# Kernel tuning notes

Measured on AMD Instinct MI355X. Metric: run time of the kernel, lower is better.

The kernel has to match this reference:

```python
import jax, jax.numpy as jnp
import numpy as np

V, C, T, H, L, B = 32000, 1024, 1024, 16, 8, 4
HS = C // H
STD = 0.02


def _layernorm(x, g, b, eps=1e-5):
    m = jnp.mean(x, axis=-1, keepdims=True)
    v = jnp.mean(jnp.square(x - m), axis=-1, keepdims=True)
    return (x - m) * jax.lax.rsqrt(v + eps) * g + b


def setup_inputs() -> dict:
    key = jax.random.key(0)
    ks = jax.random.split(key, 16)
    n = lambda k, shape: (jax.random.normal(k, shape, dtype=jnp.float32) * STD)
    return {
        "index": jax.random.randint(ks[0], (B, T), 0, V),
        "targets": jax.random.randint(ks[1], (B, T), 0, V),
        "tok_emb": n(ks[2], (V, C)),
        "pos_emb": n(ks[3], (T, C)),
        "wq": n(ks[4], (L, C, C)),
        "wk": n(ks[5], (L, C, C)),
        "wv": n(ks[6], (L, C, C)),
        "wo": n(ks[7], (L, C, C)),
        "bo": jnp.zeros((L, C), jnp.float32),
        "w1": n(ks[8], (L, C, 4 * C)),
        "b1": jnp.zeros((L, 4 * C), jnp.float32),
        "w2": n(ks[9], (L, 4 * C, C)),
        "b2": jnp.zeros((L, C), jnp.float32),
        "ln1_g": jnp.ones((L, C), jnp.float32),
        "ln1_b": jnp.zeros((L, C), jnp.float32),
        "ln2_g": jnp.ones((L, C), jnp.float32),
        "ln2_b": jnp.zeros((L, C), jnp.float32),
        "lnf_g": jnp.ones((C,), jnp.float32),
        "lnf_b": jnp.zeros((C,), jnp.float32),
        "lm_w": n(ks[10], (C, V)),
        "lm_b": jnp.zeros((V,), jnp.float32),
    }


def reference(index, targets, tok_emb, pos_emb, wq, wk, wv, wo, bo, w1, b1, w2,
              b2, ln1_g, ln1_b, ln2_g, ln2_b, lnf_g, lnf_b, lm_w, lm_b):
    b, t = index.shape
    x = tok_emb[index] + pos_emb[:t]                      # [B,T,C]
    causal = jnp.tril(jnp.ones((t, t), dtype=bool))       # tril mask
    scale = HS ** -0.5
    for l in range(L):  # fixed small layer loop
        q = (x @ wq[l]).reshape(b, t, H, HS)
        k = (x @ wk[l]).reshape(b, t, H, HS)
        v = (x @ wv[l]).reshape(b, t, H, HS)
        scores = jnp.einsum('bqhd,bkhd->bhqk', q, k) * scale
        scores = jnp.where(causal, scores, -jnp.inf)
        w = jax.nn.softmax(scores, axis=-1)               # dropout p=0 -> identity
        att = jnp.einsum('bhqk,bkhd->bqhd', w, v).reshape(b, t, C)
        x = _layernorm(x + att @ wo[l] + bo[l], ln1_g[l], ln1_b[l])
        h = jax.nn.relu(x @ w1[l] + b1[l])
        x = _layernorm(x + h @ w2[l] + b2[l], ln2_g[l], ln2_b[l])
    x = _layernorm(x, lnf_g, lnf_b)
    logits = (x @ lm_w + lm_b).reshape(b * t, V)
    logp = jax.nn.log_softmax(logits, axis=-1)
    loss = -jnp.take_along_axis(logp, targets.reshape(-1, 1), axis=1).mean()
    return logits, loss
```

## Files before the change

### kernel.cpp

```cpp
#include <hip/hip_runtime.h>

typedef unsigned short u16;
typedef __attribute__((ext_vector_type(4))) float f32x4;
typedef __attribute__((ext_vector_type(8))) short s16x8;

static constexpr int V = 32000;
static constexpr int C = 1024;
static constexpr int T = 1024;
static constexpr int H = 16;
static constexpr int L = 8;
static constexpr int B = 4;
static constexpr int HS = 64;
static constexpr int BT = B * T;
static constexpr int C4 = 4 * C;
static constexpr int C3 = 3 * C;

__device__ __forceinline__ u16 f2bf(float f) {
  union { float f; unsigned u; } v; v.f = f;
  unsigned r = v.u + 0x7fffu + ((v.u >> 16) & 1u);
  return (u16)(r >> 16);
}

__device__ __forceinline__ void gload16(const u16* g, u16* l) {
  __builtin_amdgcn_global_load_lds(
      (const __attribute__((address_space(1))) void*)g,
      (__attribute__((address_space(3))) void*)l, 16, 0, 0);
}

__device__ __forceinline__ float blockReduceSum(float v) {
  __shared__ float red[4];
  int lane = threadIdx.x & 63, w = threadIdx.x >> 6;
#pragma unroll
  for (int m = 32; m >= 1; m >>= 1) v += __shfl_xor(v, m, 64);
  if (lane == 0) red[w] = v;
  __syncthreads();
  float r = red[0] + red[1] + red[2] + red[3];
  __syncthreads();
  return r;
}

__global__ __launch_bounds__(256) void k_embed(
    const int* __restrict__ idx, const float* __restrict__ tok,
    const float* __restrict__ pos, float* __restrict__ x, u16* __restrict__ xb) {
  int bt = blockIdx.x;
  int t = bt & (T - 1);
  int row = idx[bt];
  const float* te = tok + (size_t)row * C;
  const float* pe = pos + (size_t)t * C;
  float* xo = x + (size_t)bt * C;
  u16* xbo = xb + (size_t)bt * C;
  for (int c = threadIdx.x; c < C; c += 256) {
    float v = te[c] + pe[c];
    xo[c] = v;
    xbo[c] = f2bf(v);
  }
}

__global__ __launch_bounds__(256) void k_transpose(
    const float* __restrict__ W, u16* __restrict__ Wt, int K, int N,
    size_t sW, size_t sWt) {
  __shared__ float tile[64][65];
  const float* Wz = W + sW * blockIdx.z;
  u16* Wtz = Wt + sWt * blockIdx.z;
  int n0 = blockIdx.x * 64, k0 = blockIdx.y * 64;
  int tc = threadIdx.x & 63, tr = threadIdx.x >> 6;
#pragma unroll
  for (int i = 0; i < 16; ++i) {
    int r = tr + i * 4;
    tile[r][tc] = Wz[(size_t)(k0 + r) * N + (n0 + tc)];
  }
  __syncthreads();
#pragma unroll
  for (int i = 0; i < 16; ++i) {
    int r = tr + i * 4;
    Wtz[(size_t)(n0 + r) * K + (k0 + tc)] = f2bf(tile[tc][r]);
  }
}

__global__ __launch_bounds__(256) void k_vtrans(
    const u16* __restrict__ qkv, u16* __restrict__ vt) {
  __shared__ u16 tile[64][72];
  int bid = blockIdx.x;
  int tc = bid & 15, h = (bid >> 4) & 15, b = bid >> 8;
  int t0 = tc * 64;
  const size_t base = (size_t)b * T * C3 + 2 * C + (size_t)h * HS;
  int tid = threadIdx.x;
  int r = tid >> 3, c8 = (tid & 7) * 8;
#pragma unroll
  for (int it = 0; it < 2; ++it) {
    int row = r + it * 32;
    *(s16x8*)&tile[row][c8] =
        *(const s16x8*)&qkv[base + (size_t)(t0 + row) * C3 + c8];
  }
  __syncthreads();
  const size_t vbase = (size_t)(b * H + h) * HS * T + t0;
#pragma unroll
  for (int it = 0; it < 2; ++it) {
    int d = (tid >> 3) + it * 32;
    s16x8 o;
#pragma unroll
    for (int j = 0; j < 8; ++j) o[j] = (short)tile[c8 + j][d];
    *(s16x8*)&vt[vbase + (size_t)d * T + c8] = o;
  }
}

template <int OUT_BF16, int RELU, int HAS_BIAS, int HAS_RES>
__global__ __launch_bounds__(256, 2) void k_gemm(
    const u16* __restrict__ A, const u16* __restrict__ Bt,
    const float* __restrict__ bias, const float* __restrict__ Res,
    float* __restrict__ Cf, u16* __restrict__ Cb, int M, int N, int K) {
  __shared__ u16 As[128 * 32];
  __shared__ u16 Bs[128 * 32];
  int tid = threadIdx.x;
  int lane = tid & 63, wid = tid >> 6;
  int lm = lane & 15, lg = lane >> 4;
  int wm = wid >> 1, wn = wid & 1;

  unsigned nbx = gridDim.x;
  unsigned nwg = nbx * gridDim.y;
  unsigned orig = blockIdx.y * nbx + blockIdx.x;
  unsigned f = ((nwg & 7u) == 0u) ? (orig & 7u) * (nwg >> 3) + (orig >> 3) : orig;
  int mb = (int)(f / nbx) * 128, nb = (int)(f % nbx) * 128;

  f32x4 acc[4][4];
#pragma unroll
  for (int i = 0; i < 4; ++i)
#pragma unroll
    for (int j = 0; j < 4; ++j) acc[i][j] = f32x4{0.f, 0.f, 0.f, 0.f};

  int r0 = tid >> 2, q0 = tid & 3;
  int r1 = (256 + tid) >> 2, q1 = tid & 3;
  const u16* a0 = A + (size_t)(mb + r0) * K + q0 * 8;
  const u16* a1 = A + (size_t)(mb + r1) * K + q1 * 8;
  const u16* b0 = Bt + (size_t)(nb + r0) * K + q0 * 8;
  const u16* b1 = Bt + (size_t)(nb + r1) * K + q1 * 8;
  u16* lA0 = &As[wid * 512];
  u16* lA1 = &As[2048 + wid * 512];
  u16* lB0 = &Bs[wid * 512];
  u16* lB1 = &Bs[2048 + wid * 512];

  int nK = K >> 5;
  for (int kb = 0; kb < nK; ++kb) {
    __syncthreads();
    int ko = kb * 32;
    gload16(a0 + ko, lA0);
    gload16(a1 + ko, lA1);
    gload16(b0 + ko, lB0);
    gload16(b1 + ko, lB1);
    __syncthreads();
    s16x8 af[4], bfr[4];
#pragma unroll
    for (int m = 0; m < 4; ++m)
      af[m] = *(const s16x8*)&As[(wm * 64 + m * 16 + lm) * 32 + lg * 8];
#pragma unroll
    for (int n = 0; n < 4; ++n)
      bfr[n] = *(const s16x8*)&Bs[(wn * 64 + n * 16 + lm) * 32 + lg * 8];
#pragma unroll
    for (int m = 0; m < 4; ++m)
#pragma unroll
      for (int n = 0; n < 4; ++n)
        acc[m][n] = __builtin_amdgcn_mfma_f32_16x16x32_bf16(af[m], bfr[n],
                                                            acc[m][n], 0, 0, 0);
  }
#pragma unroll
  for (int m = 0; m < 4; ++m) {
#pragma unroll
    for (int n = 0; n < 4; ++n) {
      int col = nb + wn * 64 + n * 16 + lm;
      float bv = HAS_BIAS ? bias[col] : 0.0f;
#pragma unroll
      for (int r = 0; r < 4; ++r) {
        int row = mb + wm * 64 + m * 16 + lg * 4 + r;
        float v = acc[m][n][r] + bv;
        if (HAS_RES) v += Res[(size_t)row * N + col];
        if (RELU) v = v > 0.f ? v : 0.f;
        if (OUT_BF16)
          Cb[(size_t)row * N + col] = f2bf(v);
        else
          Cf[(size_t)row * N + col] = v;
      }
    }
  }
}

template <int OUT_BF16, int RELU, int HAS_BIAS, int HAS_RES>
__global__ __launch_bounds__(512) void k_gemm256(
    const u16* __restrict__ A, const u16* __restrict__ Bt,
    const float* __restrict__ bias, const float* __restrict__ Res,
    float* __restrict__ Cf, u16* __restrict__ Cb, int M, int N, int K) {
  __shared__ u16 As[2][16384];
  __shared__ u16 Bs[2][16384];
  const int tid = threadIdx.x;
  const int lane = tid & 63, wid = tid >> 6;
  const int lm = lane & 15, lg = lane >> 4;
  const int wr = wid >> 2, wc = wid & 3;

  unsigned nbx = gridDim.x;
  unsigned nwg = nbx * gridDim.y;
  unsigned orig = blockIdx.y * nbx + blockIdx.x;
  unsigned f = ((nwg & 7u) == 0u) ? (orig & 7u) * (nwg >> 3) + (orig >> 3) : orig;
  const int mb = (int)(f / nbx) * 256, nb = (int)(f % nbx) * 256;

  int aoff[4], boff[4], ldso[4];
#pragma unroll
  for (int h = 0; h < 4; ++h) {
    const int kk = h >> 1, p = h & 1;
    int rem = p * 512 + tid;
    int rblk = rem >> 6;
    int rem2 = rem & 63;
    int row16 = rem2 >> 2, psl = rem2 & 3;
    int sl = psl ^ ((row16 >> 1) & 3);
    int grow = rblk * 16 + row16;
    int gk = kk * 32 + sl * 8;
    aoff[h] = (mb + grow) * K + gk;
    boff[h] = (nb + grow) * K + gk;
    ldso[h] = kk * 8192 + p * 4096 + wid * 512;
  }
  const int lo = lm * 32 + ((lg ^ ((lm >> 1) & 3)) << 3);

  f32x4 acc[8][4];
#pragma unroll
  for (int i = 0; i < 8; ++i)
#pragma unroll
    for (int j = 0; j < 4; ++j) acc[i][j] = f32x4{0.f, 0.f, 0.f, 0.f};

  const int nK = K >> 6;
  gload16(A + aoff[0], &As[0][ldso[0]]);
  gload16(A + aoff[1], &As[0][ldso[1]]);
  gload16(Bt + boff[0], &Bs[0][ldso[0]]);
  gload16(Bt + boff[1], &Bs[0][ldso[1]]);
  gload16(A + aoff[2], &As[0][ldso[2]]);
  gload16(A + aoff[3], &As[0][ldso[3]]);
  gload16(Bt + boff[2], &Bs[0][ldso[2]]);
  gload16(Bt + boff[3], &Bs[0][ldso[3]]);
  asm volatile("s_waitcnt vmcnt(4)" ::: "memory");
  __builtin_amdgcn_s_barrier();

  for (int t = 0; t < nK; ++t) {
    const int buf = t & 1, nbuf = buf ^ 1;
    const bool pre = (t + 1 < nK);
    const int nk64 = (t + 1) * 64;
    s16x8 af[4], bfr[4];
#pragma unroll
    for (int m = 0; m < 4; ++m)
      af[m] = *(const s16x8*)&As[buf][(wr * 8 + m) * 512 + lo];
#pragma unroll
    for (int n = 0; n < 4; ++n)
      bfr[n] = *(const s16x8*)&Bs[buf][(wc * 4 + n) * 512 + lo];
    if (pre) {
      gload16(A + aoff[0] + nk64, &As[nbuf][ldso[0]]);
      gload16(A + aoff[1] + nk64, &As[nbuf][ldso[1]]);
    }
    __builtin_amdgcn_s_barrier();
    __builtin_amdgcn_s_setprio(1);
#pragma unroll
    for (int m = 0; m < 4; ++m)
#pragma unroll
      for (int n = 0; n < 4; ++n)
        acc[m][n] = __builtin_amdgcn_mfma_f32_16x16x32_bf16(af[m], bfr[n],
                                                            acc[m][n], 0, 0, 0);
    __builtin_amdgcn_s_setprio(0);
    __builtin_amdgcn_s_barrier();
#pragma unroll
    for (int m = 0; m < 4; ++m)
      af[m] = *(const s16x8*)&As[buf][(wr * 8 + 4 + m) * 512 + lo];
    if (pre) {
      gload16(Bt + boff[0] + nk64, &Bs[nbuf][ldso[0]]);
      gload16(Bt + boff[1] + nk64, &Bs[nbuf][ldso[1]]);
    }
    __builtin_amdgcn_s_barrier();
    __builtin_amdgcn_s_setprio(1);
#pragma unroll
    for (int m = 0; m < 4; ++m)
#pragma unroll
      for (int n = 0; n < 4; ++n)
        acc[m + 4][n] = __builtin_amdgcn_mfma_f32_16x16x32_bf16(
            af[m], bfr[n], acc[m + 4][n], 0, 0, 0);
    __builtin_amdgcn_s_setprio(0);
    __builtin_amdgcn_s_barrier();
#pragma unroll
    for (int m = 0; m < 4; ++m)
      af[m] = *(const s16x8*)&As[buf][8192 + (wr * 8 + m) * 512 + lo];
#pragma unroll
    for (int n = 0; n < 4; ++n)
      bfr[n] = *(const s16x8*)&Bs[buf][8192 + (wc * 4 + n) * 512 + lo];
    if (pre) {
      gload16(A + aoff[2] + nk64, &As[nbuf][ldso[2]]);
      gload16(A + aoff[3] + nk64, &As[nbuf][ldso[3]]);
      asm volatile("s_waitcnt vmcnt(6)" ::: "memory");
    } else {
      asm volatile("s_waitcnt vmcnt(0)" ::: "memory");
    }
    __builtin_amdgcn_s_barrier();
    __builtin_amdgcn_s_setprio(1);
#pragma unroll
    for (int m = 0; m < 4; ++m)
#pragma unroll
      for (int n = 0; n < 4; ++n)
        acc[m][n] = __builtin_amdgcn_mfma_f32_16x16x32_bf16(af[m], bfr[n],
                                                            acc[m][n], 0, 0, 0);
    __builtin_amdgcn_s_setprio(0);
    __builtin_amdgcn_s_barrier();
#pragma unroll
    for (int m = 0; m < 4; ++m)
      af[m] = *(const s16x8*)&As[buf][8192 + (wr * 8 + 4 + m) * 512 + lo];
    if (pre) {
      gload16(Bt + boff[2] + nk64, &Bs[nbuf][ldso[2]]);
      gload16(Bt + boff[3] + nk64, &Bs[nbuf][ldso[3]]);
      asm volatile("s_waitcnt vmcnt(4)" ::: "memory");
    }
    __builtin_amdgcn_s_barrier();
    __builtin_amdgcn_s_setprio(1);
#pragma unroll
    for (int m = 0; m < 4; ++m)
#pragma unroll
      for (int n = 0; n < 4; ++n)
        acc[m + 4][n] = __builtin_amdgcn_mfma_f32_16x16x32_bf16(
            af[m], bfr[n], acc[m + 4][n], 0, 0, 0);
    __builtin_amdgcn_s_setprio(0);
    __builtin_amdgcn_s_barrier();
  }
  float bv[4];
#pragma unroll
  for (int n = 0; n < 4; ++n)
    bv[n] = HAS_BIAS ? bias[nb + wc * 64 + n * 16 + lm] : 0.0f;
#pragma unroll
  for (int m = 0; m < 8; ++m) {
#pragma unroll
    for (int r = 0; r < 4; ++r) {
      int row = mb + wr * 128 + m * 16 + lg * 4 + r;
#pragma unroll
      for (int n = 0; n < 4; ++n) {
        int col = nb + wc * 64 + n * 16 + lm;
        float v = acc[m][n][r] + bv[n];
        if (HAS_RES) v += Res[(size_t)row * N + col];
        if (RELU) v = v > 0.f ? v : 0.f;
        if (OUT_BF16)
          Cb[(size_t)row * N + col] = f2bf(v);
        else
          Cf[(size_t)row * N + col] = v;
      }
    }
  }
}

__global__ __launch_bounds__(256) void k_attn(
    const u16* __restrict__ qkv, const u16* __restrict__ vt,
    u16* __restrict__ o) {
  constexpr int PP = 72;
  __shared__ u16 Ks[64 * 64];
  __shared__ u16 Vs[64 * 64];
  __shared__ u16 Ps[4][16 * PP];
  int bid = blockIdx.x;
  int qt = bid & 15, h = (bid >> 4) & 15, b = bid >> 8;
  int tid = threadIdx.x, lane = tid & 63, wid = tid >> 6;
  int lm = lane & 15, lg = lane >> 4;
  const size_t rowbase = (size_t)b * T * C3 + (size_t)h * HS;
  const u16* kbase = qkv + rowbase + C;
  const u16* vbase = vt + (size_t)(b * H + h) * HS * T;
  int qb = qt * 64;
  int qw = qb + wid * 16;
  const float scale = 0.125f;

  s16x8 qf[2];
#pragma unroll
  for (int s = 0; s < 2; ++s)
    qf[s] = *(const s16x8*)&qkv[rowbase + (size_t)(qw + lm) * C3 + s * 32 + lg * 8];

  float m_[4], l_[4];
  f32x4 oacc[4];
#pragma unroll
  for (int r = 0; r < 4; ++r) { m_[r] = -3e38f; l_[r] = 0.f; }
#pragma unroll
  for (int n = 0; n < 4; ++n) oacc[n] = f32x4{0.f, 0.f, 0.f, 0.f};

  const int sr = tid >> 3, scs = (tid & 7) ^ (sr & 7);
  const int swz0 = ((lg) ^ (lm & 7)) * 8;
  const int swz1 = ((4 + lg) ^ (lm & 7)) * 8;

  for (int kt = 0; kt <= qt; ++kt) {
    __syncthreads();
    gload16(kbase + (size_t)(kt * 64 + sr) * C3 + scs * 8, &Ks[wid * 512]);
    gload16(kbase + (size_t)(kt * 64 + sr + 32) * C3 + scs * 8,
            &Ks[2048 + wid * 512]);
    gload16(vbase + (size_t)sr * T + kt * 64 + scs * 8, &Vs[wid * 512]);
    gload16(vbase + (size_t)(sr + 32) * T + kt * 64 + scs * 8,
            &Vs[2048 + wid * 512]);
    __syncthreads();

    f32x4 s[4];
#pragma unroll
    for (int ch = 0; ch < 4; ++ch) s[ch] = f32x4{0.f, 0.f, 0.f, 0.f};
#pragma unroll
    for (int ch = 0; ch < 4; ++ch) {
      s16x8 k0 = *(const s16x8*)&Ks[(ch * 16 + lm) * 64 + swz0];
      s16x8 k1 = *(const s16x8*)&Ks[(ch * 16 + lm) * 64 + swz1];
      s[ch] = __builtin_amdgcn_mfma_f32_16x16x32_bf16(qf[0], k0, s[ch], 0, 0, 0);
      s[ch] = __builtin_amdgcn_mfma_f32_16x16x32_bf16(qf[1], k1, s[ch], 0, 0, 0);
    }
    if (kt == qt) {
#pragma unroll
      for (int ch = 0; ch < 4; ++ch) {
        int col = kt * 64 + ch * 16 + lm;
#pragma unroll
        for (int r = 0; r < 4; ++r) {
          int row = qw + lg * 4 + r;
          s[ch][r] = (col <= row) ? s[ch][r] * scale : -3e38f;
        }
      }
    } else {
#pragma unroll
      for (int ch = 0; ch < 4; ++ch)
#pragma unroll
        for (int r = 0; r < 4; ++r) s[ch][r] *= scale;
    }
    float rmax[4];
#pragma unroll
    for (int r = 0; r < 4; ++r)
      rmax[r] = fmaxf(fmaxf(s[0][r], s[1][r]), fmaxf(s[2][r], s[3][r]));
#pragma unroll
    for (int mm = 1; mm < 16; mm <<= 1)
#pragma unroll
      for (int r = 0; r < 4; ++r)
        rmax[r] = fmaxf(rmax[r], __shfl_xor(rmax[r], mm, 16));
    float alpha[4], rsum[4];
#pragma unroll
    for (int r = 0; r < 4; ++r) {
      float mn = fmaxf(m_[r], rmax[r]);
      alpha[r] = __expf(m_[r] - mn);
      m_[r] = mn;
      rsum[r] = 0.f;
    }
#pragma unroll
    for (int ch = 0; ch < 4; ++ch)
#pragma unroll
      for (int r = 0; r < 4; ++r) {
        float e = __expf(s[ch][r] - m_[r]);
        s[ch][r] = e;
        rsum[r] += e;
      }
#pragma unroll
    for (int mm = 1; mm < 16; mm <<= 1)
#pragma unroll
      for (int r = 0; r < 4; ++r) rsum[r] += __shfl_xor(rsum[r], mm, 16);
#pragma unroll
    for (int r = 0; r < 4; ++r) l_[r] = l_[r] * alpha[r] + rsum[r];
#pragma unroll
    for (int n = 0; n < 4; ++n)
#pragma unroll
      for (int r = 0; r < 4; ++r) oacc[n][r] *= alpha[r];
#pragma unroll
    for (int r = 0; r < 4; ++r) {
      int pr = lg * 4 + r;
#pragma unroll
      for (int ch = 0; ch < 4; ++ch)
        Ps[wid][pr * PP + ch * 16 + lm] = f2bf(s[ch][r]);
    }
    s16x8 pa0 = *(const s16x8*)&Ps[wid][lm * PP + lg * 8];
    s16x8 pa1 = *(const s16x8*)&Ps[wid][lm * PP + 32 + lg * 8];
#pragma unroll
    for (int n = 0; n < 4; ++n) {
      s16x8 v0 = *(const s16x8*)&Vs[(n * 16 + lm) * 64 + swz0];
      s16x8 v1 = *(const s16x8*)&Vs[(n * 16 + lm) * 64 + swz1];
      oacc[n] = __builtin_amdgcn_mfma_f32_16x16x32_bf16(pa0, v0, oacc[n], 0, 0, 0);
      oacc[n] = __builtin_amdgcn_mfma_f32_16x16x32_bf16(pa1, v1, oacc[n], 0, 0, 0);
    }
  }
  const size_t obase = (size_t)b * T * C + (size_t)h * HS;
  float inv[4];
#pragma unroll
  for (int r = 0; r < 4; ++r) inv[r] = 1.0f / l_[r];
#pragma unroll
  for (int n = 0; n < 4; ++n)
#pragma unroll
    for (int r = 0; r < 4; ++r)
      o[obase + (size_t)(qw + lg * 4 + r) * C + n * 16 + lm] =
          f2bf(oacc[n][r] * inv[r]);
}

__global__ __launch_bounds__(256) void k_ln(
    const float* __restrict__ in, const float* __restrict__ g,
    const float* __restrict__ bsh, float* __restrict__ xout,
    u16* __restrict__ xbout) {
  int row = blockIdx.x;
  const float* xr = in + (size_t)row * C;
  int tid = threadIdx.x;
  float vals[4];
  float s = 0.f;
#pragma unroll
  for (int i = 0; i < 4; ++i) {
    float vv = xr[tid + i * 256];
    vals[i] = vv;
    s += vv;
  }
  s = blockReduceSum(s);
  float mean = s * (1.0f / C);
  float s2 = 0.f;
#pragma unroll
  for (int i = 0; i < 4; ++i) {
    float d = vals[i] - mean;
    s2 += d * d;
  }
  s2 = blockReduceSum(s2);
  float rstd = rsqrtf(s2 * (1.0f / C) + 1e-5f);
#pragma unroll
  for (int i = 0; i < 4; ++i) {
    int c = tid + i * 256;
    float y = (vals[i] - mean) * rstd * g[c] + bsh[c];
    xout[(size_t)row * C + c] = y;
    xbout[(size_t)row * C + c] = f2bf(y);
  }
}

__global__ __launch_bounds__(256) void k_rowloss(
    const float* __restrict__ logits, const int* __restrict__ tgt,
    float* __restrict__ rowloss) {
  int row = blockIdx.x;
  const float* lr = logits + (size_t)row * V;
  const f32x4* lr4 = (const f32x4*)lr;
  int tid = threadIdx.x;
  float m = -3e38f, s = 0.f;
  for (int i = tid; i < V / 4; i += 256) {
    f32x4 v = lr4[i];
#pragma unroll
    for (int j = 0; j < 4; ++j) {
      float x = v[j];
      if (x > m) {
        s = s * __expf(m - x) + 1.f;
        m = x;
      } else {
        s += __expf(x - m);
      }
    }
  }
#pragma unroll
  for (int d = 1; d < 64; d <<= 1) {
    float mo = __shfl_xor(m, d, 64), so = __shfl_xor(s, d, 64);
    float mn = fmaxf(m, mo);
    s = s * __expf(m - mn) + so * __expf(mo - mn);
    m = mn;
  }
  __shared__ float sm[4], ss[4];
  int w = tid >> 6;
  if ((tid & 63) == 0) { sm[w] = m; ss[w] = s; }
  __syncthreads();
  if (tid == 0) {
    float M = fmaxf(fmaxf(sm[0], sm[1]), fmaxf(sm[2], sm[3]));
    float S = ss[0] * __expf(sm[0] - M) + ss[1] * __expf(sm[1] - M) +
              ss[2] * __expf(sm[2] - M) + ss[3] * __expf(sm[3] - M);
    rowloss[row] = (M + logf(S)) - lr[tgt[row]];
  }
}

__global__ __launch_bounds__(256) void k_lossreduce(
    const float* __restrict__ rowloss, float* __restrict__ out) {
  __shared__ float red[256];
  int tid = threadIdx.x;
  float s = 0.f;
  for (int i = tid; i < BT; i += 256) s += rowloss[i];
  red[tid] = s;
  __syncthreads();
  for (int m = 128; m >= 1; m >>= 1) {
    if (tid < m) red[tid] += red[tid + m];
    __syncthreads();
  }
  if (tid == 0) out[0] = red[0] * (1.0f / BT);
}

extern "C" void kernel_launch(void* const* d_in, const int* in_sizes, int n_in,
                              void* d_out, int out_size, void* d_ws,
                              size_t ws_size, hipStream_t stream) {
  (void)in_sizes; (void)n_in; (void)out_size; (void)ws_size;
  const int* index = (const int*)d_in[0];
  const int* targets = (const int*)d_in[1];
  const float* tok_emb = (const float*)d_in[2];
  const float* pos_emb = (const float*)d_in[3];
  const float* wq = (const float*)d_in[4];
  const float* wk = (const float*)d_in[5];
  const float* wv = (const float*)d_in[6];
  const float* wo = (const float*)d_in[7];
  const float* bo = (const float*)d_in[8];
  const float* w1 = (const float*)d_in[9];
  const float* b1 = (const float*)d_in[10];
  const float* w2 = (const float*)d_in[11];
  const float* b2 = (const float*)d_in[12];
  const float* ln1_g = (const float*)d_in[13];
  const float* ln1_b = (const float*)d_in[14];
  const float* ln2_g = (const float*)d_in[15];
  const float* ln2_b = (const float*)d_in[16];
  const float* lnf_g = (const float*)d_in[17];
  const float* lnf_b = (const float*)d_in[18];
  const float* lm_w = (const float*)d_in[19];
  const float* lm_b = (const float*)d_in[20];

  float* logits = (float*)d_out;
  float* loss = logits + (size_t)BT * V;

  size_t off = 0;
  auto alloc = [&](size_t bytes) -> void* {
    off = (off + 255) & ~(size_t)255;
    void* p = (void*)((char*)d_ws + off);
    off += bytes;
    return p;
  };
  u16* wqkv_t = (u16*)alloc((size_t)L * C3 * C * 2);
  u16* wo_t = (u16*)alloc((size_t)L * C * C * 2);
  u16* w1_t = (u16*)alloc((size_t)L * C * C4 * 2);
  u16* w2_t = (u16*)alloc((size_t)L * C4 * C * 2);
  u16* lmw_t = (u16*)alloc((size_t)V * C * 2);
  float* x = (float*)alloc((size_t)BT * C * 4);
  float* tmp = (float*)alloc((size_t)BT * C * 4);
  u16* xb = (u16*)alloc((size_t)BT * C * 2);
  u16* qkvb = (u16*)alloc((size_t)BT * C3 * 2);
  u16* vtb = (u16*)alloc((size_t)BT * C * 2);
  u16* attb = (u16*)alloc((size_t)BT * C * 2);
  u16* hb = (u16*)alloc((size_t)BT * C4 * 2);
  float* rowloss = (float*)alloc((size_t)BT * 4);

  dim3 blk(256);
  dim3 blk5(512);
  k_transpose<<<dim3(C / 64, C / 64, L), blk, 0, stream>>>(
      wq, wqkv_t, C, C, (size_t)C * C, (size_t)C3 * C);
  k_transpose<<<dim3(C / 64, C / 64, L), blk, 0, stream>>>(
      wk, wqkv_t + (size_t)C * C, C, C, (size_t)C * C, (size_t)C3 * C);
  k_transpose<<<dim3(C / 64, C / 64, L), blk, 0, stream>>>(
      wv, wqkv_t + (size_t)2 * C * C, C, C, (size_t)C * C, (size_t)C3 * C);
  k_transpose<<<dim3(C / 64, C / 64, L), blk, 0, stream>>>(
      wo, wo_t, C, C, (size_t)C * C, (size_t)C * C);
  k_transpose<<<dim3(C4 / 64, C / 64, L), blk, 0, stream>>>(
      w1, w1_t, C, C4, (size_t)C * C4, (size_t)C * C4);
  k_transpose<<<dim3(C / 64, C4 / 64, L), blk, 0, stream>>>(
      w2, w2_t, C4, C, (size_t)C4 * C, (size_t)C4 * C);
  k_transpose<<<dim3(V / 64, C / 64, 1), blk, 0, stream>>>(
      lm_w, lmw_t, C, V, 0, 0);

  k_embed<<<BT, blk, 0, stream>>>(index, tok_emb, pos_emb, x, xb);

  dim3 gQKV(C3 / 128, BT / 128);
  dim3 gCC(C / 128, BT / 128);
  dim3 gC4(C4 / 256, BT / 256);
  for (int l = 0; l < L; ++l) {
    const u16* wqkvt = wqkv_t + (size_t)l * C3 * C;
    const u16* wot = wo_t + (size_t)l * C * C;
    const u16* w1t = w1_t + (size_t)l * C * C4;
    const u16* w2t = w2_t + (size_t)l * C4 * C;

    k_gemm<1, 0, 0, 0><<<gQKV, blk, 0, stream>>>(
        xb, wqkvt, nullptr, nullptr, nullptr, qkvb, BT, C3, C);
    k_vtrans<<<B * H * (T / 64), blk, 0, stream>>>(qkvb, vtb);
    k_attn<<<B * H * (T / 64), blk, 0, stream>>>(qkvb, vtb, attb);
    k_gemm<0, 0, 1, 1><<<gCC, blk, 0, stream>>>(
        attb, wot, bo + (size_t)l * C, x, tmp, nullptr, BT, C, C);
    k_ln<<<BT, blk, 0, stream>>>(tmp, ln1_g + (size_t)l * C,
                                 ln1_b + (size_t)l * C, x, xb);
    k_gemm256<1, 1, 1, 0><<<gC4, blk5, 0, stream>>>(
        xb, w1t, b1 + (size_t)l * C4, nullptr, nullptr, hb, BT, C4, C);
    k_gemm<0, 0, 1, 1><<<gCC, blk, 0, stream>>>(
        hb, w2t, b2 + (size_t)l * C, x, tmp, nullptr, BT, C, C4);
    k_ln<<<BT, blk, 0, stream>>>(tmp, ln2_g + (size_t)l * C,
                                 ln2_b + (size_t)l * C, x, xb);
  }
  k_ln<<<BT, blk, 0, stream>>>(x, lnf_g, lnf_b, x, xb);
  k_gemm256<0, 0, 1, 0><<<dim3(V / 256, BT / 256), blk5, 0, stream>>>(
      xb, lmw_t, lm_b, nullptr, logits, nullptr, BT, V, C);
  k_rowloss<<<BT, blk, 0, stream>>>(logits, targets, rowloss);
  k_lossreduce<<<1, blk, 0, stream>>>(rowloss, loss);
}
```

Baseline: 2.947 ms.

## Fuse V-transpose into QKV GEMM, balance causal attention, fuse loss partials into LM head

Several ideas land together. The QKV projection now runs on the 256-tile GEMM, whose epilogue writes V directly in transposed layout, so the separate transpose kernel is gone. Attention blocks each take a pair of query tiles (p and 15-p) to even out the causal workload. The LM-head GEMM epilogue computes per-tile row max and sum-exp partials, so the row-loss kernel only reduces 125 pairs instead of rereading all logits. These remove a kernel launch and a large logits reread, at the cost of more epilogue work and extra syncs in the GEMM.

```diff
diff --git a/kernel.cpp b/kernel.cpp
--- a/kernel.cpp
+++ b/kernel.cpp
@@ -3,6 +3,7 @@
 typedef unsigned short u16;
 typedef __attribute__((ext_vector_type(4))) float f32x4;
 typedef __attribute__((ext_vector_type(8))) short s16x8;
+typedef __attribute__((ext_vector_type(4))) short s16x4;
 
 static constexpr int V = 32000;
 static constexpr int C = 1024;
@@ -77,33 +78,6 @@
   }
 }
 
-__global__ __launch_bounds__(256) void k_vtrans(
-    const u16* __restrict__ qkv, u16* __restrict__ vt) {
-  __shared__ u16 tile[64][72];
-  int bid = blockIdx.x;
-  int tc = bid & 15, h = (bid >> 4) & 15, b = bid >> 8;
-  int t0 = tc * 64;
-  const size_t base = (size_t)b * T * C3 + 2 * C + (size_t)h * HS;
-  int tid = threadIdx.x;
-  int r = tid >> 3, c8 = (tid & 7) * 8;
-#pragma unroll
-  for (int it = 0; it < 2; ++it) {
-    int row = r + it * 32;
-    *(s16x8*)&tile[row][c8] =
-        *(const s16x8*)&qkv[base + (size_t)(t0 + row) * C3 + c8];
-  }
-  __syncthreads();
-  const size_t vbase = (size_t)(b * H + h) * HS * T + t0;
-#pragma unroll
-  for (int it = 0; it < 2; ++it) {
-    int d = (tid >> 3) + it * 32;
-    s16x8 o;
-#pragma unroll
-    for (int j = 0; j < 8; ++j) o[j] = (short)tile[c8 + j][d];
-    *(s16x8*)&vt[vbase + (size_t)d * T + c8] = o;
-  }
-}
-
 template <int OUT_BF16, int RELU, int HAS_BIAS, int HAS_RES>
 __global__ __launch_bounds__(256, 2) void k_gemm(
     const u16* __restrict__ A, const u16* __restrict__ Bt,
@@ -183,11 +157,12 @@
   }
 }
 
-template <int OUT_BF16, int RELU, int HAS_BIAS, int HAS_RES>
+template <int OUT_BF16, int RELU, int HAS_BIAS, int HAS_RES, int VT, int LOSS>
 __global__ __launch_bounds__(512) void k_gemm256(
     const u16* __restrict__ A, const u16* __restrict__ Bt,
     const float* __restrict__ bias, const float* __restrict__ Res,
-    float* __restrict__ Cf, u16* __restrict__ Cb, int M, int N, int K) {
+    float* __restrict__ Cf, u16* __restrict__ Cb, u16* __restrict__ Vtp,
+    float2* __restrict__ Pp, int M, int N, int K) {
   __shared__ u16 As[2][16384];
   __shared__ u16 Bs[2][16384];
   const int tid = threadIdx.x;
@@ -320,6 +295,24 @@
     __builtin_amdgcn_s_setprio(0);
     __builtin_amdgcn_s_barrier();
   }
+  if (VT && nb >= 2 * C) {
+    int hh = ((nb - 2 * C) >> 6) + wc;
+#pragma unroll
+    for (int m = 0; m < 8; ++m) {
+      int t0 = mb + wr * 128 + m * 16 + lg * 4;
+      int bb = t0 >> 10, tt = t0 & (T - 1);
+      size_t vbase = ((size_t)(bb * H + hh) * HS) * T + tt;
+#pragma unroll
+      for (int n = 0; n < 4; ++n) {
+        int d = n * 16 + lm;
+        s16x4 pk;
+#pragma unroll
+        for (int r = 0; r < 4; ++r) pk[r] = (short)f2bf(acc[m][n][r]);
+        *(s16x4*)&Vtp[vbase + (size_t)d * T] = pk;
+      }
+    }
+    return;
+  }
   float bv[4];
 #pragma unroll
   for (int n = 0; n < 4; ++n)
@@ -342,6 +335,80 @@
       }
     }
   }
+  if (LOSS) {
+    __syncthreads();
+    float* red = (float*)&As[0][0];
+    float Mx[8][4], Sx[8][4];
+#pragma unroll
+    for (int m = 0; m < 8; ++m)
+#pragma unroll
+      for (int r = 0; r < 4; ++r) {
+        float v0 = acc[m][0][r] + bv[0];
+        float v1 = acc[m][1][r] + bv[1];
+        float v2 = acc[m][2][r] + bv[2];
+        float v3 = acc[m][3][r] + bv[3];
+        Mx[m][r] = fmaxf(fmaxf(v0, v1), fmaxf(v2, v3));
+      }
+#pragma unroll
+    for (int d = 1; d < 16; d <<= 1)
+#pragma unroll
+      for (int m = 0; m < 8; ++m)
+#pragma unroll
+        for (int r = 0; r < 4; ++r)
+          Mx[m][r] = fmaxf(Mx[m][r], __shfl_xor(Mx[m][r], d, 16));
+    if (lm == 0) {
+#pragma unroll
+      for (int m = 0; m < 8; ++m)
+#pragma unroll
+        for (int r = 0; r < 4; ++r)
+          red[(wr * 128 + m * 16 + lg * 4 + r) * 4 + wc] = Mx[m][r];
+    }
+    __syncthreads();
+#pragma unroll
+    for (int m = 0; m < 8; ++m)
+#pragma unroll
+      for (int r = 0; r < 4; ++r) {
+        int rl = wr * 128 + m * 16 + lg * 4 + r;
+        Mx[m][r] = fmaxf(fmaxf(red[rl * 4 + 0], red[rl * 4 + 1]),
+                         fmaxf(red[rl * 4 + 2], red[rl * 4 + 3]));
+      }
+    __syncthreads();
+#pragma unroll
+    for (int m = 0; m < 8; ++m)
+#pragma unroll
+      for (int r = 0; r < 4; ++r)
+        Sx[m][r] = __expf(acc[m][0][r] + bv[0] - Mx[m][r]) +
+                   __expf(acc[m][1][r] + bv[1] - Mx[m][r]) +
+                   __expf(acc[m][2][r] + bv[2] - Mx[m][r]) +
+                   __expf(acc[m][3][r] + bv[3] - Mx[m][r]);
+#pragma unroll
+    for (int d = 1; d < 16; d <<= 1)
+#pragma unroll
+      for (int m = 0; m < 8; ++m)
+#pragma unroll
+        for (int r = 0; r < 4; ++r)
+          Sx[m][r] += __shfl_xor(Sx[m][r], d, 16);
+    if (lm == 0) {
+#pragma unroll
+      for (int m = 0; m < 8; ++m)
+#pragma unroll
+        for (int r = 0; r < 4; ++r)
+          red[(wr * 128 + m * 16 + lg * 4 + r) * 4 + wc] = Sx[m][r];
+    }
+    __syncthreads();
+    if (wc == 0 && lm == 0) {
+      int nblk = nb >> 8;
+#pragma unroll
+      for (int m = 0; m < 8; ++m)
+#pragma unroll
+        for (int r = 0; r < 4; ++r) {
+          int rl = wr * 128 + m * 16 + lg * 4 + r;
+          float ss = red[rl * 4 + 0] + red[rl * 4 + 1] + red[rl * 4 + 2] +
+                     red[rl * 4 + 3];
+          Pp[(size_t)(mb + rl) * 128 + nblk] = float2{Mx[m][r], ss};
+        }
+    }
+  }
 }
 
 __global__ __launch_bounds__(256) void k_attn(
@@ -352,130 +419,132 @@
   __shared__ u16 Vs[64 * 64];
   __shared__ u16 Ps[4][16 * PP];
   int bid = blockIdx.x;
-  int qt = bid & 15, h = (bid >> 4) & 15, b = bid >> 8;
+  int p = bid & 7, h = (bid >> 3) & 15, b = bid >> 7;
   int tid = threadIdx.x, lane = tid & 63, wid = tid >> 6;
   int lm = lane & 15, lg = lane >> 4;
   const size_t rowbase = (size_t)b * T * C3 + (size_t)h * HS;
   const u16* kbase = qkv + rowbase + C;
   const u16* vbase = vt + (size_t)(b * H + h) * HS * T;
-  int qb = qt * 64;
-  int qw = qb + wid * 16;
+  const size_t obase = (size_t)b * T * C + (size_t)h * HS;
   const float scale = 0.125f;
-
-  s16x8 qf[2];
-#pragma unroll
-  for (int s = 0; s < 2; ++s)
-    qf[s] = *(const s16x8*)&qkv[rowbase + (size_t)(qw + lm) * C3 + s * 32 + lg * 8];
-
-  float m_[4], l_[4];
-  f32x4 oacc[4];
-#pragma unroll
-  for (int r = 0; r < 4; ++r) { m_[r] = -3e38f; l_[r] = 0.f; }
-#pragma unroll
-  for (int n = 0; n < 4; ++n) oacc[n] = f32x4{0.f, 0.f, 0.f, 0.f};
-
   const int sr = tid >> 3, scs = (tid & 7) ^ (sr & 7);
-  const int swz0 = ((lg) ^ (lm & 7)) * 8;
+  const int swz0 = (lg ^ (lm & 7)) * 8;
   const int swz1 = ((4 + lg) ^ (lm & 7)) * 8;
 
-  for (int kt = 0; kt <= qt; ++kt) {
-    __syncthreads();
-    gload16(kbase + (size_t)(kt * 64 + sr) * C3 + scs * 8, &Ks[wid * 512]);
-    gload16(kbase + (size_t)(kt * 64 + sr + 32) * C3 + scs * 8,
-            &Ks[2048 + wid * 512]);
-    gload16(vbase + (size_t)sr * T + kt * 64 + scs * 8, &Vs[wid * 512]);
-    gload16(vbase + (size_t)(sr + 32) * T + kt * 64 + scs * 8,
-            &Vs[2048 + wid * 512]);
-    __syncthreads();
-
-    f32x4 s[4];
-#pragma unroll
-    for (int ch = 0; ch < 4; ++ch) s[ch] = f32x4{0.f, 0.f, 0.f, 0.f};
-#pragma unroll
-    for (int ch = 0; ch < 4; ++ch) {
-      s16x8 k0 = *(const s16x8*)&Ks[(ch * 16 + lm) * 64 + swz0];
-      s16x8 k1 = *(const s16x8*)&Ks[(ch * 16 + lm) * 64 + swz1];
-      s[ch] = __builtin_amdgcn_mfma_f32_16x16x32_bf16(qf[0], k0, s[ch], 0, 0, 0);
-      s[ch] = __builtin_amdgcn_mfma_f32_16x16x32_bf16(qf[1], k1, s[ch], 0, 0, 0);
-    }
-    if (kt == qt) {
+  for (int qi = 0; qi < 2; ++qi) {
+    int qt = qi ? (15 - p) : p;
+    int qw = qt * 64 + wid * 16;
+    s16x8 qf[2];
+#pragma unroll
+    for (int s = 0; s < 2; ++s)
+      qf[s] = *(const s16x8*)&qkv[rowbase + (size_t)(qw + lm) * C3 + s * 32 +
+                                  lg * 8];
+    float m_[4], l_[4];
+    f32x4 oacc[4];
+#pragma unroll
+    for (int r = 0; r < 4; ++r) { m_[r] = -3e38f; l_[r] = 0.f; }
+#pragma unroll
+    for (int n = 0; n < 4; ++n) oacc[n] = f32x4{0.f, 0.f, 0.f, 0.f};
+
+    for (int kt = 0; kt <= qt; ++kt) {
+      __syncthreads();
+      gload16(kbase + (size_t)(kt * 64 + sr) * C3 + scs * 8, &Ks[wid * 512]);
+      gload16(kbase + (size_t)(kt * 64 + sr + 32) * C3 + scs * 8,
+              &Ks[2048 + wid * 512]);
+      gload16(vbase + (size_t)sr * T + kt * 64 + scs * 8, &Vs[wid * 512]);
+      gload16(vbase + (size_t)(sr + 32) * T + kt * 64 + scs * 8,
+              &Vs[2048 + wid * 512]);
+      __syncthreads();
+
+      f32x4 s[4];
 #pragma unroll
       for (int ch = 0; ch < 4; ++ch) {
-        int col = kt * 64 + ch * 16 + lm;
+        s16x8 k0 = *(const s16x8*)&Ks[(ch * 16 + lm) * 64 + swz0];
+        s16x8 k1 = *(const s16x8*)&Ks[(ch * 16 + lm) * 64 + swz1];
+        s[ch] = f32x4{0.f, 0.f, 0.f, 0.f};
+        s[ch] = __builtin_amdgcn_mfma_f32_16x16x32_bf16(qf[0], k0, s[ch], 0, 0, 0);
+        s[ch] = __builtin_amdgcn_mfma_f32_16x16x32_bf16(qf[1], k1, s[ch], 0, 0, 0);
+      }
+      if (kt == qt) {
+#pragma unroll
+        for (int ch = 0; ch < 4; ++ch) {
+          int col = kt * 64 + ch * 16 + lm;
+#pragma unroll
+          for (int r = 0; r < 4; ++r) {
+            int row = qw + lg * 4 + r;
+            s[ch][r] = (col <= row) ? s[ch][r] * scale : -3e38f;
+          }
+        }
+      } else {
+#pragma unroll
+        for (int ch = 0; ch < 4; ++ch)
+#pragma unroll
+          for (int r = 0; r < 4; ++r) s[ch][r] *= scale;
+      }
+      float rmax[4];
+#pragma unroll
+      for (int r = 0; r < 4; ++r)
+        rmax[r] = fmaxf(fmaxf(s[0][r], s[1][r]), fmaxf(s[2][r], s[3][r]));
+#pragma unroll
+      for (int mm = 1; mm < 16; mm <<= 1)
+#pragma unroll
+        for (int r = 0; r < 4; ++r)
+          rmax[r] = fmaxf(rmax[r], __shfl_xor(rmax[r], mm, 16));
+      float alpha[4], rsum[4];
+#pragma unroll
+      for (int r = 0; r < 4; ++r) {
+        float mn = fmaxf(m_[r], rmax[r]);
+        alpha[r] = __expf(m_[r] - mn);
+        m_[r] = mn;
+        rsum[r] = 0.f;
+      }
+#pragma unroll
+      for (int ch = 0; ch < 4; ++ch)
 #pragma unroll
         for (int r = 0; r < 4; ++r) {
-          int row = qw + lg * 4 + r;
-          s[ch][r] = (col <= row) ? s[ch][r] * scale : -3e38f;
+          float e = __expf(s[ch][r] - m_[r]);
+          s[ch][r] = e;
+          rsum[r] += e;
         }
-      }
-    } else {
-#pragma unroll
-      for (int ch = 0; ch < 4; ++ch)
-#pragma unroll
-        for (int r = 0; r < 4; ++r) s[ch][r] *= scale;
-    }
-    float rmax[4];
-#pragma unroll
-    for (int r = 0; r < 4; ++r)
-      rmax[r] = fmaxf(fmaxf(s[0][r], s[1][r]), fmaxf(s[2][r], s[3][r]));
-#pragma unroll
-    for (int mm = 1; mm < 16; mm <<= 1)
+#pragma unroll
+      for (int mm = 1; mm < 16; mm <<= 1)
+#pragma unroll
+        for (int r = 0; r < 4; ++r) rsum[r] += __shfl_xor(rsum[r], mm, 16);
+#pragma unroll
+      for (int r = 0; r < 4; ++r) l_[r] = l_[r] * alpha[r] + rsum[r];
+#pragma unroll
+      for (int n = 0; n < 4; ++n)
+#pragma unroll
+        for (int r = 0; r < 4; ++r) oacc[n][r] *= alpha[r];
+#pragma unroll
+      for (int r = 0; r < 4; ++r) {
+        int pr = lg * 4 + r;
+#pragma unroll
+        for (int ch = 0; ch < 4; ++ch)
+          Ps[wid][pr * PP + ch * 16 + lm] = f2bf(s[ch][r]);
+      }
+      s16x8 pa0 = *(const s16x8*)&Ps[wid][lm * PP + lg * 8];
+      s16x8 pa1 = *(const s16x8*)&Ps[wid][lm * PP + 32 + lg * 8];
+#pragma unroll
+      for (int n = 0; n < 4; ++n) {
+        s16x8 v0 = *(const s16x8*)&Vs[(n * 16 + lm) * 64 + swz0];
+        s16x8 v1 = *(const s16x8*)&Vs[(n * 16 + lm) * 64 + swz1];
+        oacc[n] =
+            __builtin_amdgcn_mfma_f32_16x16x32_bf16(pa0, v0, oacc[n], 0, 0, 0);
+        oacc[n] =
+            __builtin_amdgcn_mfma_f32_16x16x32_bf16(pa1, v1, oacc[n], 0, 0, 0);
+      }
+    }
+    float inv[4];
+#pragma unroll
+    for (int r = 0; r < 4; ++r) inv[r] = 1.0f / l_[r];
+#pragma unroll
+    for (int n = 0; n < 4; ++n)
 #pragma unroll
       for (int r = 0; r < 4; ++r)
-        rmax[r] = fmaxf(rmax[r], __shfl_xor(rmax[r], mm, 16));
-    float alpha[4], rsum[4];
-#pragma unroll
-    for (int r = 0; r < 4; ++r) {
-      float mn = fmaxf(m_[r], rmax[r]);
-      alpha[r] = __expf(m_[r] - mn);
-      m_[r] = mn;
-      rsum[r] = 0.f;
-    }
-#pragma unroll
-    for (int ch = 0; ch < 4; ++ch)
-#pragma unroll
-      for (int r = 0; r < 4; ++r) {
-        float e = __expf(s[ch][r] - m_[r]);
-        s[ch][r] = e;
-        rsum[r] += e;
-      }
-#pragma unroll
-    for (int mm = 1; mm < 16; mm <<= 1)
-#pragma unroll
-      for (int r = 0; r < 4; ++r) rsum[r] += __shfl_xor(rsum[r], mm, 16);
-#pragma unroll
-    for (int r = 0; r < 4; ++r) l_[r] = l_[r] * alpha[r] + rsum[r];
-#pragma unroll
-    for (int n = 0; n < 4; ++n)
-#pragma unroll
-      for (int r = 0; r < 4; ++r) oacc[n][r] *= alpha[r];
-#pragma unroll
-    for (int r = 0; r < 4; ++r) {
-      int pr = lg * 4 + r;
-#pragma unroll
-      for (int ch = 0; ch < 4; ++ch)
-        Ps[wid][pr * PP + ch * 16 + lm] = f2bf(s[ch][r]);
-    }
-    s16x8 pa0 = *(const s16x8*)&Ps[wid][lm * PP + lg * 8];
-    s16x8 pa1 = *(const s16x8*)&Ps[wid][lm * PP + 32 + lg * 8];
-#pragma unroll
-    for (int n = 0; n < 4; ++n) {
-      s16x8 v0 = *(const s16x8*)&Vs[(n * 16 + lm) * 64 + swz0];
-      s16x8 v1 = *(const s16x8*)&Vs[(n * 16 + lm) * 64 + swz1];
-      oacc[n] = __builtin_amdgcn_mfma_f32_16x16x32_bf16(pa0, v0, oacc[n], 0, 0, 0);
-      oacc[n] = __builtin_amdgcn_mfma_f32_16x16x32_bf16(pa1, v1, oacc[n], 0, 0, 0);
-    }
-  }
-  const size_t obase = (size_t)b * T * C + (size_t)h * HS;
-  float inv[4];
-#pragma unroll
-  for (int r = 0; r < 4; ++r) inv[r] = 1.0f / l_[r];
-#pragma unroll
-  for (int n = 0; n < 4; ++n)
-#pragma unroll
-    for (int r = 0; r < 4; ++r)
-      o[obase + (size_t)(qw + lg * 4 + r) * C + n * 16 + lm] =
-          f2bf(oacc[n][r] * inv[r]);
+        o[obase + (size_t)(qw + lg * 4 + r) * C + n * 16 + lm] =
+            f2bf(oacc[n][r] * inv[r]);
+  }
 }
 
 __global__ __launch_bounds__(256) void k_ln(
@@ -512,26 +581,16 @@
   }
 }
 
-__global__ __launch_bounds__(256) void k_rowloss(
-    const float* __restrict__ logits, const int* __restrict__ tgt,
-    float* __restrict__ rowloss) {
+__global__ __launch_bounds__(128) void k_rowloss2(
+    const float2* __restrict__ pairs, const float* __restrict__ logits,
+    const int* __restrict__ tgt, float* __restrict__ rowloss) {
   int row = blockIdx.x;
-  const float* lr = logits + (size_t)row * V;
-  const f32x4* lr4 = (const f32x4*)lr;
   int tid = threadIdx.x;
   float m = -3e38f, s = 0.f;
-  for (int i = tid; i < V / 4; i += 256) {
-    f32x4 v = lr4[i];
-#pragma unroll
-    for (int j = 0; j < 4; ++j) {
-      float x = v[j];
-      if (x > m) {
-        s = s * __expf(m - x) + 1.f;
-        m = x;
-      } else {
-        s += __expf(x - m);
-      }
-    }
+  if (tid < 125) {
+    float2 pv = pairs[(size_t)row * 128 + tid];
+    m = pv.x;
+    s = pv.y;
   }
 #pragma unroll
   for (int d = 1; d < 64; d <<= 1) {
@@ -540,15 +599,13 @@
     s = s * __expf(m - mn) + so * __expf(mo - mn);
     m = mn;
   }
-  __shared__ float sm[4], ss[4];
-  int w = tid >> 6;
-  if ((tid & 63) == 0) { sm[w] = m; ss[w] = s; }
+  __shared__ float sm[2], ss[2];
+  if ((tid & 63) == 0) { sm[tid >> 6] = m; ss[tid >> 6] = s; }
   __syncthreads();
   if (tid == 0) {
-    float M = fmaxf(fmaxf(sm[0], sm[1]), fmaxf(sm[2], sm[3]));
-    float S = ss[0] * __expf(sm[0] - M) + ss[1] * __expf(sm[1] - M) +
-              ss[2] * __expf(sm[2] - M) + ss[3] * __expf(sm[3] - M);
-    rowloss[row] = (M + logf(S)) - lr[tgt[row]];
+    float M = fmaxf(sm[0], sm[1]);
+    float S = ss[0] * __expf(sm[0] - M) + ss[1] * __expf(sm[1] - M);
+    rowloss[row] = (M + logf(S)) - logits[(size_t)row * V + tgt[row]];
   }
 }
 
@@ -616,6 +673,7 @@
   u16* attb = (u16*)alloc((size_t)BT * C * 2);
   u16* hb = (u16*)alloc((size_t)BT * C4 * 2);
   float* rowloss = (float*)alloc((size_t)BT * 4);
+  float2* pairs = (float2*)alloc((size_t)BT * 128 * 8);
 
   dim3 blk(256);
   dim3 blk5(512);
@@ -636,7 +694,7 @@
 
   k_embed<<<BT, blk, 0, stream>>>(index, tok_emb, pos_emb, x, xb);
 
-  dim3 gQKV(C3 / 128, BT / 128);
+  dim3 gQKV(C3 / 256, BT / 256);
   dim3 gCC(C / 128, BT / 128);
   dim3 gC4(C4 / 256, BT / 256);
   for (int l = 0; l < L; ++l) {
@@ -645,24 +703,24 @@
     const u16* w1t = w1_t + (size_t)l * C * C4;
     const u16* w2t = w2_t + (size_t)l * C4 * C;
 
-    k_gemm<1, 0, 0, 0><<<gQKV, blk, 0, stream>>>(
-        xb, wqkvt, nullptr, nullptr, nullptr, qkvb, BT, C3, C);
-    k_vtrans<<<B * H * (T / 64), blk, 0, stream>>>(qkvb, vtb);
-    k_attn<<<B * H * (T / 64), blk, 0, stream>>>(qkvb, vtb, attb);
+    k_gemm256<1, 0, 0, 0, 1, 0><<<gQKV, blk5, 0, stream>>>(
+        xb, wqkvt, nullptr, nullptr, nullptr, qkvb, vtb, nullptr, BT, C3, C);
+    k_attn<<<B * H * 8, blk, 0, stream>>>(qkvb, vtb, attb);
     k_gemm<0, 0, 1, 1><<<gCC, blk, 0, stream>>>(
         attb, wot, bo + (size_t)l * C, x, tmp, nullptr, BT, C, C);
     k_ln<<<BT, blk, 0, stream>>>(tmp, ln1_g + (size_t)l * C,
                                  ln1_b + (size_t)l * C, x, xb);
-    k_gemm256<1, 1, 1, 0><<<gC4, blk5, 0, stream>>>(
-        xb, w1t, b1 + (size_t)l * C4, nullptr, nullptr, hb, BT, C4, C);
+    k_gemm256<1, 1, 1, 0, 0, 0><<<gC4, blk5, 0, stream>>>(
+        xb, w1t, b1 + (size_t)l * C4, nullptr, nullptr, hb, nullptr, nullptr,
+        BT, C4, C);
     k_gemm<0, 0, 1, 1><<<gCC, blk, 0, stream>>>(
         hb, w2t, b2 + (size_t)l * C, x, tmp, nullptr, BT, C, C4);
     k_ln<<<BT, blk, 0, stream>>>(tmp, ln2_g + (size_t)l * C,
                                  ln2_b + (size_t)l * C, x, xb);
   }
   k_ln<<<BT, blk, 0, stream>>>(x, lnf_g, lnf_b, x, xb);
-  k_gemm256<0, 0, 1, 0><<<dim3(V / 256, BT / 256), blk5, 0, stream>>>(
-      xb, lmw_t, lm_b, nullptr, logits, nullptr, BT, V, C);
-  k_rowloss<<<BT, blk, 0, stream>>>(logits, targets, rowloss);
+  k_gemm256<0, 0, 1, 0, 0, 1><<<dim3(V / 256, BT / 256), blk5, 0, stream>>>(
+      xb, lmw_t, lm_b, nullptr, logits, nullptr, nullptr, pairs, BT, V, C);
+  k_rowloss2<<<BT, dim3(128), 0, stream>>>(pairs, logits, targets, rowloss);
   k_lossreduce<<<1, blk, 0, stream>>>(rowloss, loss);
 }
```

New measurement: 2.719 ms. -7.8%, faster.
